# Kernel optimization log

Measured on AMD Instinct MI355X. Metric: run time of the kernel, lower is better.

The kernel has to match this reference:

```python
import jax, jax.numpy as jnp
import numpy as np

N_NODES = 100000
N_EDGES = 1600000
IN_FEATS = 128
HIDDEN = 128


def _graph_conv(x, W, b, src, dst, n_nodes):
    # DGL GraphConv with norm='both': out = D_in^{-1/2} * A^T * (D_out^{-1/2} * x) @ W + b
    ones = jnp.ones((src.shape[0],), dtype=x.dtype)
    deg_out = jax.ops.segment_sum(ones, src, num_segments=n_nodes)
    deg_in = jax.ops.segment_sum(ones, dst, num_segments=n_nodes)
    norm_src = jax.lax.rsqrt(jnp.clip(deg_out, 1.0))  # [N]
    norm_dst = jax.lax.rsqrt(jnp.clip(deg_in, 1.0))   # [N]
    h = x @ W                                          # [N, F_out]
    msg = h[src] * norm_src[src][:, None]              # gather by edge src: [E, F_out]
    agg = jax.ops.segment_sum(msg, dst, num_segments=n_nodes)  # scatter-add to dst
    return agg * norm_dst[:, None] + b


def setup_inputs() -> dict:
    key = jax.random.key(0)
    ks = jax.random.split(key, 9)
    x = jax.random.normal(ks[0], (N_NODES, IN_FEATS), dtype=jnp.float32)
    src = jax.random.randint(ks[1], (N_EDGES,), 0, N_NODES, dtype=jnp.int32)
    dst = jax.random.randint(ks[2], (N_EDGES,), 0, N_NODES, dtype=jnp.int32)
    s1 = 1.0 / np.sqrt(IN_FEATS)
    s2 = 1.0 / np.sqrt(HIDDEN)
    W1 = jax.random.uniform(ks[3], (IN_FEATS, HIDDEN), jnp.float32, -s1, s1)
    b1 = jnp.zeros((HIDDEN,), jnp.float32)
    W2 = jax.random.uniform(ks[4], (HIDDEN, HIDDEN), jnp.float32, -s2, s2)
    b2 = jnp.zeros((HIDDEN,), jnp.float32)
    sp = 1.0 / np.sqrt(2 * HIDDEN)
    Wp = jax.random.uniform(ks[5], (2 * HIDDEN, 1), jnp.float32, -sp, sp)
    bp = jax.random.uniform(ks[6], (1,), jnp.float32, -sp, sp)
    return {"x": x, "W1": W1, "b1": b1, "W2": W2, "b2": b2,
            "Wp": Wp, "bp": bp, "src": src, "dst": dst}


def reference(x, W1, b1, W2, b2, Wp, bp, src, dst):
    n_nodes = x.shape[0]
    h = _graph_conv(x, W1, b1, src, dst, n_nodes)
    h = jax.nn.relu(h)
    h = _graph_conv(h, W2, b2, src, dst, n_nodes)  # final node embeddings [N, H]
    # predict_links on the same edge list: cat(h[u], h[v]) -> linear -> sigmoid
    edge_h = jnp.concatenate([h[src], h[dst]], axis=1)  # [E, 2H]
    scores = jax.nn.sigmoid(edge_h @ Wp + bp)           # [E, 1]
    return scores
```

## Files before the change

### kernel.cpp

```cpp
#include <hip/hip_runtime.h>
#include <cstdint>
#include <cstddef>

#define NN 100000
#define NE 1600000
#define F  128
#define NPAD 100352
#define NBUCK 3125
#define BCAPG 768
#define NFILL 1536
#define NGEMM 1024
#define CHUNK 1042
#define GSTRIDE 16
#define NREG 49
#define RCAP 36864
#define P2SPLIT 16
#define P2J 17
#define P2MAX 2304

typedef __attribute__((ext_vector_type(8))) short bf16x8;
typedef __attribute__((ext_vector_type(4))) float f32x4;

__device__ __forceinline__ unsigned short f2bf(float f) {
    unsigned u = __float_as_uint(f);
    unsigned r = (u + 0x7fffu + ((u >> 16) & 1u)) >> 16;
    return (unsigned short)r;
}
__device__ __forceinline__ void acc_bf8s(const uint4 v, const float ns, float* acc) {
    acc[0] += __uint_as_float(v.x << 16) * ns;
    acc[1] += __uint_as_float(v.x & 0xffff0000u) * ns;
    acc[2] += __uint_as_float(v.y << 16) * ns;
    acc[3] += __uint_as_float(v.y & 0xffff0000u) * ns;
    acc[4] += __uint_as_float(v.z << 16) * ns;
    acc[5] += __uint_as_float(v.z & 0xffff0000u) * ns;
    acc[6] += __uint_as_float(v.w << 16) * ns;
    acc[7] += __uint_as_float(v.w & 0xffff0000u) * ns;
}

__global__ void setup_kernel(int* __restrict__ gCur, int* __restrict__ gRegCur,
                             int* __restrict__ gRegCurS,
                             const float* __restrict__ W2, const float* __restrict__ Wp,
                             const float* __restrict__ b2, const float* __restrict__ bp,
                             float* __restrict__ consts, float2* __restrict__ V) {
    const int g = blockIdx.x;
    const int tid = threadIdx.x;
    if (g < 13) {
        const int b = g * 256 + tid;
        if (b < NBUCK) gCur[b * GSTRIDE] = b * BCAPG;
        return;
    }
    if (g == 14) {
        if (tid < NREG) gRegCur[tid * GSTRIDE] = tid * RCAP;
        else if (tid >= 64 && tid < 64 + NREG) {
            const int r = tid - 64;
            gRegCurS[r * GSTRIDE] = r * RCAP;
        }
        return;
    }
    if (tid < 128) {
        float sa = 0.f, sc = 0.f;
        #pragma unroll 8
        for (int j = 0; j < F; ++j) {
            const float w = W2[tid * F + j];
            sa += w * Wp[j];
            sc += w * Wp[F + j];
        }
        V[tid] = make_float2(sa, sc);
    } else if (tid < 192) {
        const int l = tid - 128;
        const float2 bb = *(const float2*)&b2[2 * l];
        const float2 wa = *(const float2*)&Wp[2 * l];
        const float2 wc = *(const float2*)&Wp[F + 2 * l];
        float s = bb.x * (wa.x + wc.x) + bb.y * (wa.y + wc.y);
        #pragma unroll
        for (int m = 32; m > 0; m >>= 1) s += __shfl_xor(s, m);
        if (l == 0) consts[0] = s + bp[0];
    }
}

__global__ __launch_bounds__(256, 8)
void fill_kernel(const int* __restrict__ src, const int* __restrict__ dst,
                 int* __restrict__ gRegCur, int* __restrict__ gRegCurS,
                 int* __restrict__ gRegion, unsigned short* __restrict__ gRegionS) {
    __shared__ int sortedL[CHUNK];
    __shared__ unsigned char regOf[CHUNK];
    __shared__ int cnt[NREG], cur[NREG], base[NREG];

    const int g = blockIdx.x;
    const int tid = threadIdx.x;
    const int e0 = g * CHUNK;
    const int nCh = min(CHUNK, NE - e0);

    if (tid < NREG) cnt[tid] = 0;
    __syncthreads();
    for (int i = tid; i < nCh; i += 256)
        atomicAdd(&cnt[dst[e0 + i] >> 11], 1);
    __syncthreads();
    if (tid < NREG && cnt[tid] > 0)
        base[tid] = atomicAdd(&gRegCur[tid * GSTRIDE], cnt[tid]);
    if (tid == 0) {
        int run = 0;
        for (int r = 0; r < NREG; ++r) { cur[r] = run; run += cnt[r]; }
    }
    __syncthreads();
    for (int i = tid; i < nCh; i += 256) {
        const int s = src[e0 + i];
        const int d = dst[e0 + i];
        const int r = d >> 11;
        const int p = atomicAdd(&cur[r], 1);
        sortedL[p] = s | ((d & 0x7FF) << 17);
        regOf[p] = (unsigned char)r;
    }
    __syncthreads();
    for (int i = tid; i < nCh; i += 256) {
        const int r = regOf[i];
        const int dstAbs = base[r] + (i - (cur[r] - cnt[r]));
        if (dstAbs < (r + 1) * RCAP)
            gRegion[dstAbs] = sortedL[i];
    }
    __syncthreads();

    if (tid < NREG) cnt[tid] = 0;
    __syncthreads();
    for (int i = tid; i < nCh; i += 256)
        atomicAdd(&cnt[src[e0 + i] >> 11], 1);
    __syncthreads();
    if (tid < NREG && cnt[tid] > 0)
        base[tid] = atomicAdd(&gRegCurS[tid * GSTRIDE], cnt[tid]);
    if (tid == 0) {
        int run = 0;
        for (int r = 0; r < NREG; ++r) { cur[r] = run; run += cnt[r]; }
    }
    __syncthreads();
    for (int i = tid; i < nCh; i += 256) {
        const int s = src[e0 + i];
        const int r = s >> 11;
        const int p = atomicAdd(&cur[r], 1);
        sortedL[p] = s;
        regOf[p] = (unsigned char)r;
    }
    __syncthreads();
    for (int i = tid; i < nCh; i += 256) {
        const int r = regOf[i];
        const int dstAbs = base[r] + (i - (cur[r] - cnt[r]));
        if (dstAbs < (r + 1) * RCAP)
            gRegionS[dstAbs] = (unsigned short)(sortedL[i] & 0x7FF);
    }
}

__global__ __launch_bounds__(256, 4)
void gemm1_kernel(const float* __restrict__ in, const float* __restrict__ W,
                  unsigned short* __restrict__ out_bf) {
    __shared__ __align__(16) char A_s[8192];

    const int g    = blockIdx.x;
    const int tid  = threadIdx.x;
    const int w    = tid >> 6;
    const int lane = tid & 63;
    const int ml   = lane & 15;
    const int quad = lane >> 4;

    bf16x8 Bf[4][2];
    #pragma unroll
    for (int kb = 0; kb < 4; ++kb) {
        #pragma unroll
        for (int nb = 0; nb < 2; ++nb) {
            const int n = 32 * w + nb * 16 + ml;
            const int k0 = kb * 32 + quad * 8;
            #pragma unroll
            for (int j = 0; j < 8; ++j)
                Bf[kb][nb][j] = (short)f2bf(W[(k0 + j) * F + n]);
        }
    }

    const int nTiles = NN / 32;
    for (int tile = g; tile < nTiles; tile += NGEMM) {
        const int row0 = tile * 32;
        __syncthreads();
        #pragma unroll
        for (int c = 0; c < 2; ++c) {
            const int i2 = tid + 256 * c;
            const int m  = i2 >> 4;
            const int o  = i2 & 15;
            const float* xr = &in[(size_t)(row0 + m) * F + o * 8];
            const float4 v0 = *(const float4*)xr;
            const float4 v1 = *(const float4*)(xr + 4);
            short h8[8];
            h8[0] = (short)f2bf(v0.x); h8[1] = (short)f2bf(v0.y);
            h8[2] = (short)f2bf(v0.z); h8[3] = (short)f2bf(v0.w);
            h8[4] = (short)f2bf(v1.x); h8[5] = (short)f2bf(v1.y);
            h8[6] = (short)f2bf(v1.z); h8[7] = (short)f2bf(v1.w);
            const int kb2 = o >> 2, q2 = o & 3, ml2 = m & 15, mh2 = m >> 4;
            const int fo = (((mh2 * 4 + kb2) * 64) + q2 * 16 + ml2) * 16;
            *(bf16x8*)(A_s + fo) = *(bf16x8*)h8;
        }
        __syncthreads();

        f32x4 acc00 = {0,0,0,0}, acc01 = {0,0,0,0}, acc10 = {0,0,0,0}, acc11 = {0,0,0,0};
        #pragma unroll
        for (int kb = 0; kb < 4; ++kb) {
            const bf16x8 ah0 = *(const bf16x8*)(A_s + (kb * 64 + lane) * 16);
            const bf16x8 ah1 = *(const bf16x8*)(A_s + ((4 + kb) * 64 + lane) * 16);
            acc00 = __builtin_amdgcn_mfma_f32_16x16x32_bf16(ah0, Bf[kb][0], acc00, 0, 0, 0);
            acc01 = __builtin_amdgcn_mfma_f32_16x16x32_bf16(ah0, Bf[kb][1], acc01, 0, 0, 0);
            acc10 = __builtin_amdgcn_mfma_f32_16x16x32_bf16(ah1, Bf[kb][0], acc10, 0, 0, 0);
            acc11 = __builtin_amdgcn_mfma_f32_16x16x32_bf16(ah1, Bf[kb][1], acc11, 0, 0, 0);
        }

        #pragma unroll
        for (int mh = 0; mh < 2; ++mh) {
            #pragma unroll
            for (int nb = 0; nb < 2; ++nb) {
                const f32x4 a = (mh == 0) ? (nb == 0 ? acc00 : acc01)
                                          : (nb == 0 ? acc10 : acc11);
                const int row = row0 + mh * 16 + quad * 4;
                const int col = 32 * w + nb * 16 + ml;
                #pragma unroll
                for (int r = 0; r < 4; ++r)
                    out_bf[(size_t)(row + r) * F + col] = f2bf(a[r]);
            }
        }
    }
}

__global__ __launch_bounds__(256)
void pass2_kernel(const int* __restrict__ gRegion, const unsigned short* __restrict__ gRegionS,
                  const int* __restrict__ gRegCur, const int* __restrict__ gRegCurS,
                  int* __restrict__ gCur, int* __restrict__ srcPart,
                  float* __restrict__ norm_src) {
    __shared__ __align__(16) char smem[12544];

    const int r   = blockIdx.x / P2J;
    const int j   = blockIdx.x % P2J;
    const int tid = threadIdx.x;

    if (j == P2SPLIT) {
        int* hist = (int*)smem;
        const int total = min(gRegCurS[r * GSTRIDE] - r * RCAP, RCAP);
        for (int t = tid; t < 2048; t += 256) hist[t] = 0;
        __syncthreads();
        for (int i = tid; i < total; i += 256)
            atomicAdd(&hist[gRegionS[r * RCAP + i]], 1);
        __syncthreads();
        const int nlo = r * 2048;
        for (int t = tid; t < 2048; t += 256) {
            const int n = nlo + t;
            if (n < NN) norm_src[n] = rsqrtf((float)max(hist[t], 1));
        }
        return;
    }

    int* sortedL = (int*)smem;
    unsigned char* fbOf = (unsigned char*)(smem + 9216);
    int* cnt  = (int*)(smem + 11520);
    int* cur  = cnt + 64;
    int* base = cur + 64;

    const int total = min(gRegCur[r * GSTRIDE] - r * RCAP, RCAP);
    const int per = (total + P2SPLIT - 1) / P2SPLIT;
    const int i0 = j * per;
    const int i1 = min(total, i0 + per);
    const int n = i1 - i0;

    if (tid < 64) cnt[tid] = 0;
    __syncthreads();

    int v[9];
    #pragma unroll
    for (int k = 0; k < 9; ++k) {
        const int i = tid + k * 256;
        if (i < n) {
            const int vv = gRegion[r * RCAP + i0 + i];
            v[k] = vv;
            atomicAdd(&cnt[vv >> 22], 1);
        }
    }
    __syncthreads();
    if (tid < 64 && cnt[tid] > 0)
        base[tid] = atomicAdd(&gCur[(r * 64 + tid) * GSTRIDE], cnt[tid]);
    if (tid == 0) {
        int run = 0;
        for (int f = 0; f < 64; ++f) { cur[f] = run; run += cnt[f]; }
    }
    __syncthreads();
    #pragma unroll
    for (int k = 0; k < 9; ++k) {
        const int i = tid + k * 256;
        if (i < n) {
            const int fb = v[k] >> 22;
            const int p = atomicAdd(&cur[fb], 1);
            sortedL[p] = v[k] & 0x3FFFFF;
            fbOf[p] = (unsigned char)fb;
        }
    }
    __syncthreads();
    for (int i = tid; i < n; i += 256) {
        const int fb = fbOf[i];
        const int dstAbs = base[fb] + (i - (cur[fb] - cnt[fb]));
        if (dstAbs < (r * 64 + fb + 1) * BCAPG)
            srcPart[dstAbs] = sortedL[i];
    }
}

__global__ __launch_bounds__(256)
void gather_sort_kernel(const unsigned short* __restrict__ hs,
                        int* __restrict__ srcPart, const int* __restrict__ gCur,
                        const float* __restrict__ norm_src, const float* __restrict__ bias,
                        const float2* __restrict__ V, float2* __restrict__ uw,
                        int* __restrict__ offs, int* __restrict__ ends,
                        float* __restrict__ norm_dst) {
    __shared__ int cnt[32];
    __shared__ int loc[32];
    __shared__ int cur[32];
    __shared__ int sortedL[BCAPG];

    const int b   = blockIdx.x;
    const int tid = threadIdx.x;
    const int nlo = b * 32;
    const int nCnt = min(32, NN - nlo);
    const int eBase = b * BCAPG;
    const int total = min(gCur[b * GSTRIDE] - eBase, BCAPG);

    if (tid < 32) cnt[tid] = 0;
    __syncthreads();
    for (int i = tid; i < total; i += 256)
        atomicAdd(&cnt[(srcPart[eBase + i] >> 17) & 31], 1);
    __syncthreads();
    if (tid < 32) loc[tid] = cnt[tid];
    __syncthreads();
    for (int off = 1; off < 32; off <<= 1) {
        int v = 0;
        if (tid < 32 && tid >= off) v = loc[tid - off];
        __syncthreads();
        if (tid < 32) loc[tid] += v;
        __syncthreads();
    }
    if (tid < 32) cur[tid] = loc[tid] - cnt[tid];
    if (tid < nCnt) {
        const int st = eBase + loc[tid] - cnt[tid];
        offs[nlo + tid] = st;
        ends[nlo + tid] = st + cnt[tid];
        norm_dst[nlo + tid] = rsqrtf((float)max(cnt[tid], 1));
    }
    __syncthreads();
    for (int i = tid; i < total; i += 256) {
        const int v = srcPart[eBase + i];
        const int r = atomicAdd(&cur[(v >> 17) & 31], 1);
        sortedL[r] = v & 0x1FFFF;
    }
    __syncthreads();
    for (int i = tid; i < total; i += 256)
        srcPart[eBase + i] = sortedL[i];

    const int w  = tid >> 6;
    const int l  = tid & 63;
    const int q  = l >> 4;
    const int c8 = (l & 15) * 8;
    float bb[8];
    *(float4*)&bb[0] = *(const float4*)&bias[c8];
    *(float4*)&bb[4] = *(const float4*)&bias[c8 + 4];
    float2 Vl[8];
    #pragma unroll
    for (int k = 0; k < 8; ++k) Vl[k] = V[c8 + k];

    const int nhEnd = min((w + 1) * 8, nCnt);
    for (int nh = w * 8; nh < nhEnd; ++nh) {
        const int end = loc[nh];
        const int beg = end - cnt[nh];
        float acc[8] = {0.f, 0.f, 0.f, 0.f, 0.f, 0.f, 0.f, 0.f};
        int j = beg;
        for (; j + 16 <= end; j += 16) {
            const int s0 = sortedL[j + q];
            const int s1 = sortedL[j + 4 + q];
            const int s2 = sortedL[j + 8 + q];
            const int s3 = sortedL[j + 12 + q];
            const float ns0 = norm_src[s0];
            const float ns1 = norm_src[s1];
            const float ns2 = norm_src[s2];
            const float ns3 = norm_src[s3];
            const uint4 v0 = *(const uint4*)&hs[(size_t)s0 * F + c8];
            const uint4 v1 = *(const uint4*)&hs[(size_t)s1 * F + c8];
            const uint4 v2 = *(const uint4*)&hs[(size_t)s2 * F + c8];
            const uint4 v3 = *(const uint4*)&hs[(size_t)s3 * F + c8];
            acc_bf8s(v0, ns0, acc);
            acc_bf8s(v1, ns1, acc);
            acc_bf8s(v2, ns2, acc);
            acc_bf8s(v3, ns3, acc);
        }
        for (; j + 8 <= end; j += 8) {
            const int s0 = sortedL[j + q];
            const int s1 = sortedL[j + 4 + q];
            const float ns0 = norm_src[s0];
            const float ns1 = norm_src[s1];
            const uint4 v0 = *(const uint4*)&hs[(size_t)s0 * F + c8];
            const uint4 v1 = *(const uint4*)&hs[(size_t)s1 * F + c8];
            acc_bf8s(v0, ns0, acc);
            acc_bf8s(v1, ns1, acc);
        }
        for (; j + 4 <= end; j += 4) {
            const int s = sortedL[j + q];
            const float ns = norm_src[s];
            const uint4 v = *(const uint4*)&hs[(size_t)s * F + c8];
            acc_bf8s(v, ns, acc);
        }
        if (j + q < end) {
            const int s = sortedL[j + q];
            const float ns = norm_src[s];
            const uint4 v = *(const uint4*)&hs[(size_t)s * F + c8];
            acc_bf8s(v, ns, acc);
        }
        #pragma unroll
        for (int k = 0; k < 8; ++k) {
            acc[k] += __shfl_xor(acc[k], 16);
            acc[k] += __shfl_xor(acc[k], 32);
        }

        const int n = nlo + nh;
        const float nd = rsqrtf((float)max(cnt[nh], 1));
        float pa = 0.f, pc = 0.f;
        #pragma unroll
        for (int k = 0; k < 8; ++k) {
            const float ok = fmaxf(acc[k] * nd + bb[k], 0.f);
            pa += ok * Vl[k].x;
            pc += ok * Vl[k].y;
        }
        #pragma unroll
        for (int m = 1; m <= 8; m <<= 1) {
            pa += __shfl_xor(pa, m);
            pc += __shfl_xor(pc, m);
        }
        if (l == 0) {
            const float ns = norm_src[n];
            uw[n] = make_float2(ns * pa, ns * pc);
        }
    }
}

__global__ void ac_kernel(const float2* __restrict__ uw, const int* __restrict__ sorted_src,
                          const int* __restrict__ offs, const int* __restrict__ ends,
                          const float* __restrict__ norm_dst,
                          float* __restrict__ A, float* __restrict__ C, int nN) {
    const int n = blockIdx.x * blockDim.x + threadIdx.x;
    if (n >= nN) return;
    const int beg = offs[n];
    const int end = ends[n];
    float su = 0.f, sw = 0.f;
    int j = beg;
    for (; j + 2 <= end; j += 2) {
        const float2 t0 = uw[sorted_src[j]];
        const float2 t1 = uw[sorted_src[j + 1]];
        su += t0.x + t1.x;
        sw += t0.y + t1.y;
    }
    if (j < end) {
        const float2 t = uw[sorted_src[j]];
        su += t.x;
        sw += t.y;
    }
    const float nd = norm_dst[n];
    A[n] = nd * su;
    C[n] = nd * sw;
}

__global__ void score_kernel(const float* __restrict__ A, const float* __restrict__ C,
                             const int4* __restrict__ src4, const int4* __restrict__ dst4,
                             const float* __restrict__ consts, float4* __restrict__ out4,
                             int nE4) {
    const int i = blockIdx.x * blockDim.x + threadIdx.x;
    if (i < nE4) {
        const int4 s = src4[i];
        const int4 d = dst4[i];
        const float cc = consts[0];
        float4 o;
        o.x = 1.f / (1.f + __expf(-(A[s.x] + C[d.x] + cc)));
        o.y = 1.f / (1.f + __expf(-(A[s.y] + C[d.y] + cc)));
        o.z = 1.f / (1.f + __expf(-(A[s.z] + C[d.z] + cc)));
        o.w = 1.f / (1.f + __expf(-(A[s.w] + C[d.w] + cc)));
        out4[i] = o;
    }
}

extern "C" void kernel_launch(void* const* d_in, const int* in_sizes, int n_in,
                              void* d_out, int out_size, void* d_ws, size_t ws_size,
                              hipStream_t stream) {
    const float* x  = (const float*)d_in[0];
    const float* W1 = (const float*)d_in[1];
    const float* b1 = (const float*)d_in[2];
    const float* W2 = (const float*)d_in[3];
    const float* b2 = (const float*)d_in[4];
    const float* Wp = (const float*)d_in[5];
    const float* bp = (const float*)d_in[6];
    const int*   src = (const int*)d_in[7];
    const int*   dst = (const int*)d_in[8];
    float* out = (float*)d_out;

    float* ws        = (float*)d_ws;
    float* norm_src  = ws;
    float* bufA      = ws + NPAD;
    float* bufC      = ws + 2 * NPAD;
    float* norm_dst  = ws + 3 * NPAD;
    int*   offs      = (int*)(ws + 4 * NPAD);
    int*   ends      = offs + NPAD;
    int*   gCur      = ends + NPAD;
    int*   gRegCur   = gCur + 50176;
    int*   gRegCurS  = gRegCur + 1024;
    float* consts    = (float*)(gRegCurS + 1024);
    float2* V        = (float2*)(consts + 16);
    float2* uw       = V + 128;
    int*   srcPart   = (int*)(uw + NN);
    unsigned short* hs_bf = (unsigned short*)(srcPart + (size_t)NBUCK * BCAPG);
    int*   gRegion   = (int*)(hs_bf + (size_t)NN * F);
    unsigned short* gRegionS = (unsigned short*)(gRegion + (size_t)NREG * RCAP);

    setup_kernel<<<15, 256, 0, stream>>>(gCur, gRegCur, gRegCurS, W2, Wp, b2, bp, consts, V);

    fill_kernel<<<NFILL, 256, 0, stream>>>(src, dst, gRegCur, gRegCurS, gRegion, gRegionS);

    gemm1_kernel<<<NGEMM, 256, 0, stream>>>(x, W1, hs_bf);

    pass2_kernel<<<NREG * P2J, 256, 0, stream>>>(gRegion, gRegionS, gRegCur, gRegCurS,
                                                 gCur, srcPart, norm_src);

    gather_sort_kernel<<<NBUCK, 256, 0, stream>>>(hs_bf, srcPart, gCur, norm_src, b1,
                                                  V, uw, offs, ends, norm_dst);

    ac_kernel<<<(NN + 255) / 256, 256, 0, stream>>>(uw, srcPart, offs, ends, norm_dst,
                                                    bufA, bufC, NN);

    score_kernel<<<(NE / 4 + 255) / 256, 256, 0, stream>>>(bufA, bufC, (const int4*)src,
                                                           (const int4*)dst, consts,
                                                           (float4*)out, NE / 4);
}
```

Baseline: 330.4 us.

## Fold source-degree normalization into GEMM epilogue and persist gather blocks

New measurement: 341.9 us. 3.5% more time.

```diff
diff --git a/kernel.cpp b/kernel.cpp
--- a/kernel.cpp
+++ b/kernel.cpp
@@ -10,6 +10,7 @@
 #define BCAPG 768
 #define NFILL 1536
 #define NGEMM 1024
+#define NGATH 1563
 #define CHUNK 1042
 #define GSTRIDE 16
 #define NREG 49
@@ -26,15 +27,15 @@
     unsigned r = (u + 0x7fffu + ((u >> 16) & 1u)) >> 16;
     return (unsigned short)r;
 }
-__device__ __forceinline__ void acc_bf8s(const uint4 v, const float ns, float* acc) {
-    acc[0] += __uint_as_float(v.x << 16) * ns;
-    acc[1] += __uint_as_float(v.x & 0xffff0000u) * ns;
-    acc[2] += __uint_as_float(v.y << 16) * ns;
-    acc[3] += __uint_as_float(v.y & 0xffff0000u) * ns;
-    acc[4] += __uint_as_float(v.z << 16) * ns;
-    acc[5] += __uint_as_float(v.z & 0xffff0000u) * ns;
-    acc[6] += __uint_as_float(v.w << 16) * ns;
-    acc[7] += __uint_as_float(v.w & 0xffff0000u) * ns;
+__device__ __forceinline__ void acc_bf8(const uint4 v, float* acc) {
+    acc[0] += __uint_as_float(v.x << 16);
+    acc[1] += __uint_as_float(v.x & 0xffff0000u);
+    acc[2] += __uint_as_float(v.y << 16);
+    acc[3] += __uint_as_float(v.y & 0xffff0000u);
+    acc[4] += __uint_as_float(v.z << 16);
+    acc[5] += __uint_as_float(v.z & 0xffff0000u);
+    acc[6] += __uint_as_float(v.w << 16);
+    acc[7] += __uint_as_float(v.w & 0xffff0000u);
 }
 
 __global__ void setup_kernel(int* __restrict__ gCur, int* __restrict__ gRegCur,
@@ -150,6 +151,7 @@
 
 __global__ __launch_bounds__(256, 4)
 void gemm1_kernel(const float* __restrict__ in, const float* __restrict__ W,
+                  const float* __restrict__ norm_src,
                   unsigned short* __restrict__ out_bf) {
     __shared__ __align__(16) char A_s[8192];
 
@@ -209,15 +211,18 @@
 
         #pragma unroll
         for (int mh = 0; mh < 2; ++mh) {
+            const int rowb = row0 + mh * 16 + quad * 4;
+            float ns[4];
+            #pragma unroll
+            for (int r = 0; r < 4; ++r) ns[r] = norm_src[rowb + r];
             #pragma unroll
             for (int nb = 0; nb < 2; ++nb) {
                 const f32x4 a = (mh == 0) ? (nb == 0 ? acc00 : acc01)
                                           : (nb == 0 ? acc10 : acc11);
-                const int row = row0 + mh * 16 + quad * 4;
                 const int col = 32 * w + nb * 16 + ml;
                 #pragma unroll
                 for (int r = 0; r < 4; ++r)
-                    out_bf[(size_t)(row + r) * F + col] = f2bf(a[r]);
+                    out_bf[(size_t)(rowb + r) * F + col] = f2bf(a[r] * ns[r]);
             }
         }
     }
@@ -314,44 +319,7 @@
     __shared__ int cur[32];
     __shared__ int sortedL[BCAPG];
 
-    const int b   = blockIdx.x;
     const int tid = threadIdx.x;
-    const int nlo = b * 32;
-    const int nCnt = min(32, NN - nlo);
-    const int eBase = b * BCAPG;
-    const int total = min(gCur[b * GSTRIDE] - eBase, BCAPG);
-
-    if (tid < 32) cnt[tid] = 0;
-    __syncthreads();
-    for (int i = tid; i < total; i += 256)
-        atomicAdd(&cnt[(srcPart[eBase + i] >> 17) & 31], 1);
-    __syncthreads();
-    if (tid < 32) loc[tid] = cnt[tid];
-    __syncthreads();
-    for (int off = 1; off < 32; off <<= 1) {
-        int v = 0;
-        if (tid < 32 && tid >= off) v = loc[tid - off];
-        __syncthreads();
-        if (tid < 32) loc[tid] += v;
-        __syncthreads();
-    }
-    if (tid < 32) cur[tid] = loc[tid] - cnt[tid];
-    if (tid < nCnt) {
-        const int st = eBase + loc[tid] - cnt[tid];
-        offs[nlo + tid] = st;
-        ends[nlo + tid] = st + cnt[tid];
-        norm_dst[nlo + tid] = rsqrtf((float)max(cnt[tid], 1));
-    }
-    __syncthreads();
-    for (int i = tid; i < total; i += 256) {
-        const int v = srcPart[eBase + i];
-        const int r = atomicAdd(&cur[(v >> 17) & 31], 1);
-        sortedL[r] = v & 0x1FFFF;
-    }
-    __syncthreads();
-    for (int i = tid; i < total; i += 256)
-        srcPart[eBase + i] = sortedL[i];
-
     const int w  = tid >> 6;
     const int l  = tid & 63;
     const int q  = l >> 4;
@@ -363,75 +331,106 @@
     #pragma unroll
     for (int k = 0; k < 8; ++k) Vl[k] = V[c8 + k];
 
-    const int nhEnd = min((w + 1) * 8, nCnt);
-    for (int nh = w * 8; nh < nhEnd; ++nh) {
-        const int end = loc[nh];
-        const int beg = end - cnt[nh];
-        float acc[8] = {0.f, 0.f, 0.f, 0.f, 0.f, 0.f, 0.f, 0.f};
-        int j = beg;
-        for (; j + 16 <= end; j += 16) {
-            const int s0 = sortedL[j + q];
-            const int s1 = sortedL[j + 4 + q];
-            const int s2 = sortedL[j + 8 + q];
-            const int s3 = sortedL[j + 12 + q];
-            const float ns0 = norm_src[s0];
-            const float ns1 = norm_src[s1];
-            const float ns2 = norm_src[s2];
-            const float ns3 = norm_src[s3];
-            const uint4 v0 = *(const uint4*)&hs[(size_t)s0 * F + c8];
-            const uint4 v1 = *(const uint4*)&hs[(size_t)s1 * F + c8];
-            const uint4 v2 = *(const uint4*)&hs[(size_t)s2 * F + c8];
-            const uint4 v3 = *(const uint4*)&hs[(size_t)s3 * F + c8];
-            acc_bf8s(v0, ns0, acc);
-            acc_bf8s(v1, ns1, acc);
-            acc_bf8s(v2, ns2, acc);
-            acc_bf8s(v3, ns3, acc);
-        }
-        for (; j + 8 <= end; j += 8) {
-            const int s0 = sortedL[j + q];
-            const int s1 = sortedL[j + 4 + q];
-            const float ns0 = norm_src[s0];
-            const float ns1 = norm_src[s1];
-            const uint4 v0 = *(const uint4*)&hs[(size_t)s0 * F + c8];
-            const uint4 v1 = *(const uint4*)&hs[(size_t)s1 * F + c8];
-            acc_bf8s(v0, ns0, acc);
-            acc_bf8s(v1, ns1, acc);
-        }
-        for (; j + 4 <= end; j += 4) {
-            const int s = sortedL[j + q];
-            const float ns = norm_src[s];
-            const uint4 v = *(const uint4*)&hs[(size_t)s * F + c8];
-            acc_bf8s(v, ns, acc);
-        }
-        if (j + q < end) {
-            const int s = sortedL[j + q];
-            const float ns = norm_src[s];
-            const uint4 v = *(const uint4*)&hs[(size_t)s * F + c8];
-            acc_bf8s(v, ns, acc);
-        }
-        #pragma unroll
-        for (int k = 0; k < 8; ++k) {
-            acc[k] += __shfl_xor(acc[k], 16);
-            acc[k] += __shfl_xor(acc[k], 32);
-        }
-
-        const int n = nlo + nh;
-        const float nd = rsqrtf((float)max(cnt[nh], 1));
-        float pa = 0.f, pc = 0.f;
-        #pragma unroll
-        for (int k = 0; k < 8; ++k) {
-            const float ok = fmaxf(acc[k] * nd + bb[k], 0.f);
-            pa += ok * Vl[k].x;
-            pc += ok * Vl[k].y;
-        }
-        #pragma unroll
-        for (int m = 1; m <= 8; m <<= 1) {
-            pa += __shfl_xor(pa, m);
-            pc += __shfl_xor(pc, m);
-        }
-        if (l == 0) {
-            const float ns = norm_src[n];
-            uw[n] = make_float2(ns * pa, ns * pc);
+    for (int b = blockIdx.x; b < NBUCK; b += NGATH) {
+        __syncthreads();
+        const int nlo = b * 32;
+        const int nCnt = min(32, NN - nlo);
+        const int eBase = b * BCAPG;
+        const int total = min(gCur[b * GSTRIDE] - eBase, BCAPG);
+
+        if (tid < 32) cnt[tid] = 0;
+        __syncthreads();
+        for (int i = tid; i < total; i += 256)
+            atomicAdd(&cnt[(srcPart[eBase + i] >> 17) & 31], 1);
+        __syncthreads();
+        if (tid < 32) loc[tid] = cnt[tid];
+        __syncthreads();
+        for (int off = 1; off < 32; off <<= 1) {
+            int v = 0;
+            if (tid < 32 && tid >= off) v = loc[tid - off];
+            __syncthreads();
+            if (tid < 32) loc[tid] += v;
+            __syncthreads();
+        }
+        if (tid < 32) cur[tid] = loc[tid] - cnt[tid];
+        if (tid < nCnt) {
+            const int st = eBase + loc[tid] - cnt[tid];
+            offs[nlo + tid] = st;
+            ends[nlo + tid] = st + cnt[tid];
+            norm_dst[nlo + tid] = rsqrtf((float)max(cnt[tid], 1));
+        }
+        __syncthreads();
+        for (int i = tid; i < total; i += 256) {
+            const int v = srcPart[eBase + i];
+            const int r = atomicAdd(&cur[(v >> 17) & 31], 1);
+            sortedL[r] = v & 0x1FFFF;
+        }
+        __syncthreads();
+        for (int i = tid; i < total; i += 256)
+            srcPart[eBase + i] = sortedL[i];
+
+        const int nhEnd = min((w + 1) * 8, nCnt);
+        for (int nh = w * 8; nh < nhEnd; ++nh) {
+            const int end = loc[nh];
+            const int beg = end - cnt[nh];
+            float acc[8] = {0.f, 0.f, 0.f, 0.f, 0.f, 0.f, 0.f, 0.f};
+            int j = beg;
+            for (; j + 16 <= end; j += 16) {
+                const int s0 = sortedL[j + q];
+                const int s1 = sortedL[j + 4 + q];
+                const int s2 = sortedL[j + 8 + q];
+                const int s3 = sortedL[j + 12 + q];
+                const uint4 v0 = *(const uint4*)&hs[(size_t)s0 * F + c8];
+                const uint4 v1 = *(const uint4*)&hs[(size_t)s1 * F + c8];
+                const uint4 v2 = *(const uint4*)&hs[(size_t)s2 * F + c8];
+                const uint4 v3 = *(const uint4*)&hs[(size_t)s3 * F + c8];
+                acc_bf8(v0, acc);
+                acc_bf8(v1, acc);
+                acc_bf8(v2, acc);
+                acc_bf8(v3, acc);
+            }
+            for (; j + 8 <= end; j += 8) {
+                const int s0 = sortedL[j + q];
+                const int s1 = sortedL[j + 4 + q];
+                const uint4 v0 = *(const uint4*)&hs[(size_t)s0 * F + c8];
+                const uint4 v1 = *(const uint4*)&hs[(size_t)s1 * F + c8];
+                acc_bf8(v0, acc);
+                acc_bf8(v1, acc);
+            }
+            for (; j + 4 <= end; j += 4) {
+                const int s = sortedL[j + q];
+                const uint4 v = *(const uint4*)&hs[(size_t)s * F + c8];
+                acc_bf8(v, acc);
+            }
+            if (j + q < end) {
+                const int s = sortedL[j + q];
+                const uint4 v = *(const uint4*)&hs[(size_t)s * F + c8];
+                acc_bf8(v, acc);
+            }
+            #pragma unroll
+            for (int k = 0; k < 8; ++k) {
+                acc[k] += __shfl_xor(acc[k], 16);
+                acc[k] += __shfl_xor(acc[k], 32);
+            }
+
+            const int n = nlo + nh;
+            const float nd = rsqrtf((float)max(cnt[nh], 1));
+            float pa = 0.f, pc = 0.f;
+            #pragma unroll
+            for (int k = 0; k < 8; ++k) {
+                const float ok = fmaxf(acc[k] * nd + bb[k], 0.f);
+                pa += ok * Vl[k].x;
+                pc += ok * Vl[k].y;
+            }
+            #pragma unroll
+            for (int m = 1; m <= 8; m <<= 1) {
+                pa += __shfl_xor(pa, m);
+                pc += __shfl_xor(pc, m);
+            }
+            if (l == 0) {
+                const float ns = norm_src[n];
+                uw[n] = make_float2(ns * pa, ns * pc);
+            }
         }
     }
 }
@@ -516,12 +515,12 @@
 
     fill_kernel<<<NFILL, 256, 0, stream>>>(src, dst, gRegCur, gRegCurS, gRegion, gRegionS);
 
-    gemm1_kernel<<<NGEMM, 256, 0, stream>>>(x, W1, hs_bf);
-
     pass2_kernel<<<NREG * P2J, 256, 0, stream>>>(gRegion, gRegionS, gRegCur, gRegCurS,
                                                  gCur, srcPart, norm_src);
 
-    gather_sort_kernel<<<NBUCK, 256, 0, stream>>>(hs_bf, srcPart, gCur, norm_src, b1,
+    gemm1_kernel<<<NGEMM, 256, 0, stream>>>(x, W1, norm_src, hs_bf);
+
+    gather_sort_kernel<<<NGATH, 256, 0, stream>>>(hs_bf, srcPart, gCur, norm_src, b1,
                                                   V, uw, offs, ends, norm_dst);
 
     ac_kernel<<<(NN + 255) / 256, 256, 0, stream>>>(uw, srcPart, offs, ends, norm_dst,
```

## Fuse edge fill with GEMM1, use wave-shuffle scans and subgroup AC reduction

Applied to the files above, without the earlier changes.

Result: faster. 285.1 us (-13.7%).

```diff
diff --git a/kernel.cpp b/kernel.cpp
--- a/kernel.cpp
+++ b/kernel.cpp
@@ -8,9 +8,7 @@
 #define NPAD 100352
 #define NBUCK 3125
 #define BCAPG 768
-#define NFILL 1536
-#define NGEMM 1024
-#define CHUNK 1042
+#define CHUNK 4167
 #define GSTRIDE 16
 #define NREG 49
 #define RCAP 36864
@@ -78,83 +76,88 @@
     }
 }
 
-__global__ __launch_bounds__(256, 8)
-void fill_kernel(const int* __restrict__ src, const int* __restrict__ dst,
-                 int* __restrict__ gRegCur, int* __restrict__ gRegCurS,
-                 int* __restrict__ gRegion, unsigned short* __restrict__ gRegionS) {
-    __shared__ int sortedL[CHUNK];
-    __shared__ unsigned char regOf[CHUNK];
-    __shared__ int cnt[NREG], cur[NREG], base[NREG];
+__global__ __launch_bounds__(256, 3)
+void gemm1_fill_kernel(const float* __restrict__ in, const float* __restrict__ W,
+                       unsigned short* __restrict__ out_bf,
+                       const int* __restrict__ src, const int* __restrict__ dst,
+                       int* __restrict__ gRegCur, int* __restrict__ gRegCurS,
+                       int* __restrict__ gRegion, unsigned short* __restrict__ gRegionS) {
+    __shared__ __align__(16) char smem[21504];
 
     const int g = blockIdx.x;
     const int tid = threadIdx.x;
-    const int e0 = g * CHUNK;
-    const int nCh = min(CHUNK, NE - e0);
-
-    if (tid < NREG) cnt[tid] = 0;
-    __syncthreads();
-    for (int i = tid; i < nCh; i += 256)
-        atomicAdd(&cnt[dst[e0 + i] >> 11], 1);
-    __syncthreads();
-    if (tid < NREG && cnt[tid] > 0)
-        base[tid] = atomicAdd(&gRegCur[tid * GSTRIDE], cnt[tid]);
-    if (tid == 0) {
-        int run = 0;
-        for (int r = 0; r < NREG; ++r) { cur[r] = run; run += cnt[r]; }
-    }
-    __syncthreads();
-    for (int i = tid; i < nCh; i += 256) {
-        const int s = src[e0 + i];
-        const int d = dst[e0 + i];
-        const int r = d >> 11;
-        const int p = atomicAdd(&cur[r], 1);
-        sortedL[p] = s | ((d & 0x7FF) << 17);
-        regOf[p] = (unsigned char)r;
-    }
-    __syncthreads();
-    for (int i = tid; i < nCh; i += 256) {
-        const int r = regOf[i];
-        const int dstAbs = base[r] + (i - (cur[r] - cnt[r]));
-        if (dstAbs < (r + 1) * RCAP)
-            gRegion[dstAbs] = sortedL[i];
-    }
-    __syncthreads();
-
-    if (tid < NREG) cnt[tid] = 0;
-    __syncthreads();
-    for (int i = tid; i < nCh; i += 256)
-        atomicAdd(&cnt[src[e0 + i] >> 11], 1);
-    __syncthreads();
-    if (tid < NREG && cnt[tid] > 0)
-        base[tid] = atomicAdd(&gRegCurS[tid * GSTRIDE], cnt[tid]);
-    if (tid == 0) {
-        int run = 0;
-        for (int r = 0; r < NREG; ++r) { cur[r] = run; run += cnt[r]; }
-    }
-    __syncthreads();
-    for (int i = tid; i < nCh; i += 256) {
-        const int s = src[e0 + i];
-        const int r = s >> 11;
-        const int p = atomicAdd(&cur[r], 1);
-        sortedL[p] = s;
-        regOf[p] = (unsigned char)r;
-    }
-    __syncthreads();
-    for (int i = tid; i < nCh; i += 256) {
-        const int r = regOf[i];
-        const int dstAbs = base[r] + (i - (cur[r] - cnt[r]));
-        if (dstAbs < (r + 1) * RCAP)
-            gRegionS[dstAbs] = (unsigned short)(sortedL[i] & 0x7FF);
-    }
-}
-
-__global__ __launch_bounds__(256, 4)
-void gemm1_kernel(const float* __restrict__ in, const float* __restrict__ W,
-                  unsigned short* __restrict__ out_bf) {
-    __shared__ __align__(16) char A_s[8192];
-
-    const int g    = blockIdx.x;
-    const int tid  = threadIdx.x;
+
+    if (g & 1) {
+        int* sortedL = (int*)smem;
+        unsigned char* regOf = (unsigned char*)(sortedL + CHUNK);
+        int* cnt  = (int*)(smem + 20840);
+        int* cur  = cnt + NREG;
+        int* base = cur + NREG;
+
+        const int e0 = (g >> 1) * CHUNK;
+        const int nCh = min(CHUNK, NE - e0);
+
+        if (tid < NREG) cnt[tid] = 0;
+        __syncthreads();
+        for (int i = tid; i < nCh; i += 256)
+            atomicAdd(&cnt[dst[e0 + i] >> 11], 1);
+        __syncthreads();
+        if (tid < NREG && cnt[tid] > 0)
+            base[tid] = atomicAdd(&gRegCur[tid * GSTRIDE], cnt[tid]);
+        if (tid == 0) {
+            int run = 0;
+            for (int r = 0; r < NREG; ++r) { cur[r] = run; run += cnt[r]; }
+        }
+        __syncthreads();
+        for (int i = tid; i < nCh; i += 256) {
+            const int s = src[e0 + i];
+            const int d = dst[e0 + i];
+            const int r = d >> 11;
+            const int p = atomicAdd(&cur[r], 1);
+            sortedL[p] = s | ((d & 0x7FF) << 17);
+            regOf[p] = (unsigned char)r;
+        }
+        __syncthreads();
+        for (int i = tid; i < nCh; i += 256) {
+            const int r = regOf[i];
+            const int dstAbs = base[r] + (i - (cur[r] - cnt[r]));
+            if (dstAbs < (r + 1) * RCAP)
+                gRegion[dstAbs] = sortedL[i];
+        }
+        __syncthreads();
+
+        if (tid < NREG) cnt[tid] = 0;
+        __syncthreads();
+        for (int i = tid; i < nCh; i += 256)
+            atomicAdd(&cnt[src[e0 + i] >> 11], 1);
+        __syncthreads();
+        if (tid < NREG && cnt[tid] > 0)
+            base[tid] = atomicAdd(&gRegCurS[tid * GSTRIDE], cnt[tid]);
+        if (tid == 0) {
+            int run = 0;
+            for (int r = 0; r < NREG; ++r) { cur[r] = run; run += cnt[r]; }
+        }
+        __syncthreads();
+        for (int i = tid; i < nCh; i += 256) {
+            const int s = src[e0 + i];
+            const int r = s >> 11;
+            const int p = atomicAdd(&cur[r], 1);
+            sortedL[p] = s;
+            regOf[p] = (unsigned char)r;
+        }
+        __syncthreads();
+        for (int i = tid; i < nCh; i += 256) {
+            const int r = regOf[i];
+            const int dstAbs = base[r] + (i - (cur[r] - cnt[r]));
+            if (dstAbs < (r + 1) * RCAP)
+                gRegionS[dstAbs] = (unsigned short)(sortedL[i] & 0x7FF);
+        }
+        return;
+    }
+
+    char* A_s = smem;
+
+    const int gid  = g >> 1;
     const int w    = tid >> 6;
     const int lane = tid & 63;
     const int ml   = lane & 15;
@@ -174,7 +177,7 @@
     }
 
     const int nTiles = NN / 32;
-    for (int tile = g; tile < nTiles; tile += NGEMM) {
+    for (int tile = gid; tile < nTiles; tile += 384) {
         const int row0 = tile * 32;
         __syncthreads();
         #pragma unroll
@@ -317,7 +320,6 @@
     const int b   = blockIdx.x;
     const int tid = threadIdx.x;
     const int nlo = b * 32;
-    const int nCnt = min(32, NN - nlo);
     const int eBase = b * BCAPG;
     const int total = min(gCur[b * GSTRIDE] - eBase, BCAPG);
 
@@ -326,21 +328,23 @@
     for (int i = tid; i < total; i += 256)
         atomicAdd(&cnt[(srcPart[eBase + i] >> 17) & 31], 1);
     __syncthreads();
-    if (tid < 32) loc[tid] = cnt[tid];
-    __syncthreads();
-    for (int off = 1; off < 32; off <<= 1) {
-        int v = 0;
-        if (tid < 32 && tid >= off) v = loc[tid - off];
-        __syncthreads();
-        if (tid < 32) loc[tid] += v;
-        __syncthreads();
-    }
-    if (tid < 32) cur[tid] = loc[tid] - cnt[tid];
-    if (tid < nCnt) {
-        const int st = eBase + loc[tid] - cnt[tid];
-        offs[nlo + tid] = st;
-        ends[nlo + tid] = st + cnt[tid];
-        norm_dst[nlo + tid] = rsqrtf((float)max(cnt[tid], 1));
+    if (tid < 64) {
+        const int l32 = tid & 31;
+        const int c = cnt[l32];
+        int v = c;
+        #pragma unroll
+        for (int off = 1; off < 32; off <<= 1) {
+            const int t = __shfl_up(v, off, 32);
+            if (l32 >= off) v += t;
+        }
+        if (tid < 32) {
+            loc[tid] = v;
+            cur[tid] = v - c;
+            const int st = eBase + v - c;
+            offs[nlo + tid] = st;
+            ends[nlo + tid] = st + c;
+            norm_dst[nlo + tid] = rsqrtf((float)max(c, 1));
+        }
     }
     __syncthreads();
     for (int i = tid; i < total; i += 256) {
@@ -363,7 +367,7 @@
     #pragma unroll
     for (int k = 0; k < 8; ++k) Vl[k] = V[c8 + k];
 
-    const int nhEnd = min((w + 1) * 8, nCnt);
+    const int nhEnd = (w + 1) * 8;
     for (int nh = w * 8; nh < nhEnd; ++nh) {
         const int end = loc[nh];
         const int beg = end - cnt[nh];
@@ -436,30 +440,30 @@
     }
 }
 
-__global__ void ac_kernel(const float2* __restrict__ uw, const int* __restrict__ sorted_src,
-                          const int* __restrict__ offs, const int* __restrict__ ends,
-                          const float* __restrict__ norm_dst,
-                          float* __restrict__ A, float* __restrict__ C, int nN) {
-    const int n = blockIdx.x * blockDim.x + threadIdx.x;
-    if (n >= nN) return;
+__global__ __launch_bounds__(256, 8)
+void ac_kernel(const float2* __restrict__ uw, const int* __restrict__ sorted_src,
+               const int* __restrict__ offs, const int* __restrict__ ends,
+               const float* __restrict__ norm_dst,
+               float* __restrict__ A, float* __restrict__ C) {
+    const int tid = threadIdx.x;
+    const int n   = blockIdx.x * 32 + (tid >> 3);
+    const int sub = tid & 7;
     const int beg = offs[n];
     const int end = ends[n];
-    float su = 0.f, sw = 0.f;
-    int j = beg;
-    for (; j + 2 <= end; j += 2) {
-        const float2 t0 = uw[sorted_src[j]];
-        const float2 t1 = uw[sorted_src[j + 1]];
-        su += t0.x + t1.x;
-        sw += t0.y + t1.y;
-    }
-    if (j < end) {
+    float sx = 0.f, sy = 0.f;
+    for (int j = beg + sub; j < end; j += 8) {
         const float2 t = uw[sorted_src[j]];
-        su += t.x;
-        sw += t.y;
-    }
-    const float nd = norm_dst[n];
-    A[n] = nd * su;
-    C[n] = nd * sw;
+        sx += t.x;
+        sy += t.y;
+    }
+    sx += __shfl_xor(sx, 1); sy += __shfl_xor(sy, 1);
+    sx += __shfl_xor(sx, 2); sy += __shfl_xor(sy, 2);
+    sx += __shfl_xor(sx, 4); sy += __shfl_xor(sy, 4);
+    if (sub == 0) {
+        const float nd = norm_dst[n];
+        A[n] = nd * sx;
+        C[n] = nd * sy;
+    }
 }
 
 __global__ void score_kernel(const float* __restrict__ A, const float* __restrict__ C,
@@ -514,9 +518,8 @@
 
     setup_kernel<<<15, 256, 0, stream>>>(gCur, gRegCur, gRegCurS, W2, Wp, b2, bp, consts, V);
 
-    fill_kernel<<<NFILL, 256, 0, stream>>>(src, dst, gRegCur, gRegCurS, gRegion, gRegionS);
-
-    gemm1_kernel<<<NGEMM, 256, 0, stream>>>(x, W1, hs_bf);
+    gemm1_fill_kernel<<<768, 256, 0, stream>>>(x, W1, hs_bf, src, dst,
+                                               gRegCur, gRegCurS, gRegion, gRegionS);
 
     pass2_kernel<<<NREG * P2J, 256, 0, stream>>>(gRegion, gRegionS, gRegCur, gRegCurS,
                                                  gCur, srcPart, norm_src);
@@ -524,8 +527,8 @@
     gather_sort_kernel<<<NBUCK, 256, 0, stream>>>(hs_bf, srcPart, gCur, norm_src, b1,
                                                   V, uw, offs, ends, norm_dst);
 
-    ac_kernel<<<(NN + 255) / 256, 256, 0, stream>>>(uw, srcPart, offs, ends, norm_dst,
-                                                    bufA, bufC, NN);
+    ac_kernel<<<NBUCK, 256, 0, stream>>>(uw, srcPart, offs, ends, norm_dst,
+                                         bufA, bufC);
 
     score_kernel<<<(NE / 4 + 255) / 256, 256, 0, stream>>>(bufA, bufC, (const int4*)src,
                                                            (const int4*)dst, consts,
```
